# Optimization experiments

Hardware: AMD Instinct MI355X
Metric: run time of the kernel (lower is better)

The kernel has to match this reference:

```python
import jax, jax.numpy as jnp
import numpy as np

NUM_JOINTS = 24
NUM_THETAS = NUM_JOINTS * 3  # 72
NUM_VERTS = 6890
NUM_BETAS = 10
BATCH = 512

SMPL_PARENTS = np.array([0, 0, 0, 0, 1, 2, 3, 4, 5, 6, 7, 8, 9, 9, 9,
                         12, 13, 14, 16, 17, 18, 19, 20, 21], dtype=np.int32)


def setup_inputs() -> dict:
    key = jax.random.key(0)
    ks = jax.random.split(key, 6)
    x = jax.random.normal(ks[0], (BATCH, NUM_THETAS + NUM_BETAS), dtype=jnp.float32) * 0.3
    v_template = jax.random.normal(ks[1], (NUM_VERTS, 3), dtype=jnp.float32) * 0.3
    shapedirs = jax.random.normal(ks[2], (NUM_BETAS, NUM_VERTS * 3), dtype=jnp.float32) * 0.01
    posedirs = jax.random.normal(ks[3], (207, NUM_VERTS * 3), dtype=jnp.float32) * 0.001
    Jr = jax.random.uniform(ks[4], (NUM_VERTS, NUM_JOINTS), dtype=jnp.float32)
    J_regressor = Jr / jnp.sum(Jr, axis=0, keepdims=True)
    W = jax.random.uniform(ks[5], (NUM_VERTS, NUM_JOINTS), dtype=jnp.float32)
    lbs_weights = W / jnp.sum(W, axis=1, keepdims=True)  # rows sum to 1 (skinning weights)
    parents = jnp.asarray(SMPL_PARENTS)
    return {"x": x, "v_template": v_template, "shapedirs": shapedirs,
            "J_regressor": J_regressor, "posedirs": posedirs,
            "lbs_weights": lbs_weights, "parents": parents}


def batch_rodrigues(theta):
    # theta: [N,3] axis-angle -> [N,3,3] rotation matrices
    angle = jnp.linalg.norm(theta + 1e-8, axis=1, keepdims=True)  # [N,1]
    r = theta / angle                                              # [N,3] unit axis
    cos = jnp.cos(angle)[..., None]                                # [N,1,1]
    sin = jnp.sin(angle)[..., None]
    outer = r[:, :, None] * r[:, None, :]                          # [N,3,3]
    rx, ry, rz = r[:, 0], r[:, 1], r[:, 2]
    zero = jnp.zeros_like(rx)
    K = jnp.stack([zero, -rz, ry,
                   rz, zero, -rx,
                   -ry, rx, zero], axis=1).reshape(-1, 3, 3)       # skew-symmetric
    eye = jnp.eye(3, dtype=theta.dtype)
    return cos * eye + (1.0 - cos) * outer + sin * K


def global_rigid_transformation(Rs, J, parents):
    # Rs: [B,24,3,3], J: [B,24,3] -> A: [B,24,4,4]
    B = Rs.shape[0]
    dtype = Rs.dtype
    bottom = jnp.broadcast_to(jnp.array([0, 0, 0, 1], dtype=dtype), (B, 1, 4))

    def make_A(R, t):  # R:[B,3,3], t:[B,3]
        Rt = jnp.concatenate([R, t[:, :, None]], axis=2)  # [B,3,4]
        return jnp.concatenate([Rt, bottom], axis=1)       # [B,4,4]

    parents = np.asarray(parents)
    results = [make_A(Rs[:, 0], J[:, 0])]
    for i in range(1, NUM_JOINTS):
        t_rel = J[:, i] - J[:, parents[i]]
        A_here = make_A(Rs[:, i], t_rel)
        results.append(jnp.matmul(results[parents[i]], A_here))
    results = jnp.stack(results, axis=1)  # [B,24,4,4]

    Js_w0 = jnp.concatenate([J, jnp.zeros((B, NUM_JOINTS, 1), dtype=dtype)], axis=2)  # [B,24,4]
    init_bone = jnp.einsum('bjpq,bjq->bjp', results, Js_w0)                           # [B,24,4]
    A = results - jnp.pad(init_bone[..., None], ((0, 0), (0, 0), (0, 0), (3, 0)))
    return A


def reference(x, v_template, shapedirs, J_regressor, posedirs, lbs_weights, parents):
    B = x.shape[0]
    thetas = x[:, :NUM_THETAS]
    betas = x[:, NUM_THETAS:]

    # shape blendshapes
    v_shaped = (betas @ shapedirs).reshape(B, NUM_VERTS, 3) + v_template  # [B,V,3]

    J = jnp.einsum('bvc,vj->bjc', v_shaped, J_regressor)  # [B,24,3]

    # pose rotations + pose blendshapes
    Rs = batch_rodrigues(thetas.reshape(-1, 3)).reshape(B, NUM_JOINTS, 3, 3)
    pose_feature = (Rs[:, 1:] - jnp.eye(3, dtype=x.dtype)).reshape(B, 207)
    v_posed = (pose_feature @ posedirs).reshape(B, NUM_VERTS, 3) + v_shaped

    # kinematic chain
    A = global_rigid_transformation(Rs, J, parents)  # [B,24,4,4]

    # linear blend skinning
    T = jnp.einsum('vj,bjpq->bvpq', lbs_weights, A)  # [B,V,4,4]
    v_posed_homo = jnp.concatenate(
        [v_posed, jnp.ones((B, NUM_VERTS, 1), dtype=x.dtype)], axis=2)  # [B,V,4]
    verts = jnp.einsum('bvpq,bvq->bvp', T, v_posed_homo)[:, :, :3]
    return verts
```

## Files before the change

kernel.cpp:

```cpp
#include <hip/hip_runtime.h>

#define NUM_JOINTS 24
#define NUM_VERTS  6890
#define NUM_COORDS (NUM_VERTS * 3)
#define NUM_BETAS  10
#define KTOT       217
#define KPAD       224
#define BATCH      512
#define VPAD       6912

#define WS_SJP  0
#define WS_XBF  85536
#define WS_DBF  142880
#define WS_WHBF 2465312
#define WS_AH   2575904
#define WS_AL   2706976

typedef __attribute__((ext_vector_type(8))) short short8;
typedef __attribute__((ext_vector_type(4))) float f32x4;

__device__ inline unsigned short f2bf(float f) {
    union { float f; unsigned u; } c; c.f = f;
    unsigned u = c.u;
    u += 0x7fffu + ((u >> 16) & 1u);
    return (unsigned short)(u >> 16);
}
__device__ inline float bf2f(unsigned short h) {
    union { unsigned u; float f; } c; c.u = ((unsigned)h) << 16;
    return c.f;
}

struct PBShm {
    float Rs[4][24][9];
    float Jl[4][24][3];
    float Rg[4][24][9];
    float tg[4][24][3];
    float As[4][24][12];
};

__global__ __launch_bounds__(256) void k_prep(const float* __restrict__ Jr,
                                              const float* __restrict__ sd,
                                              const float* __restrict__ pd,
                                              const float* __restrict__ vt,
                                              const float* __restrict__ w,
                                              float* __restrict__ ws) {
    __shared__ __align__(16) unsigned char smem[28928];
    const int t   = blockIdx.x;
    const int tid = threadIdx.x;
    unsigned short* whbf = (unsigned short*)(ws + WS_WHBF);
    unsigned short* dbf  = (unsigned short*)(ws + WS_DBF);

    if (t < 27) {
        const int v = t * 256 + tid;
        const bool ok = (v < NUM_VERTS);
        unsigned short row[32];
        #pragma unroll
        for (int j = 0; j < 32; ++j)
            row[j] = f2bf((ok && j < 24) ? w[v * 24 + j] : 0.f);
        #pragma unroll
        for (int i = 0; i < 4; ++i)
            *(float4*)(whbf + (size_t)v * 32 + i * 8) = *(const float4*)(&row[i * 8]);
    } else if (t < 351) {
        unsigned* L = (unsigned*)smem;
        const int c0   = (t - 27) * 64;
        const int lane = tid & 63;
        const int grp  = tid >> 6;
        const int c    = c0 + lane;
        const bool cv  = (c < NUM_COORDS);
        #pragma unroll 4
        for (int i = 0; i < 28; ++i) {
            const int p  = i * 4 + grp;
            const int k0 = 2 * p, k1 = k0 + 1;
            float v0 = 0.f, v1 = 0.f;
            if (cv) {
                v0 = (k0 < 10) ? sd[(size_t)k0 * NUM_COORDS + c]
                   : (k0 < KTOT) ? pd[(size_t)(k0 - 10) * NUM_COORDS + c] : 0.f;
                v1 = (k1 < 10) ? sd[(size_t)k1 * NUM_COORDS + c]
                   : (k1 < KTOT) ? pd[(size_t)(k1 - 10) * NUM_COORDS + c] : 0.f;
            }
            L[lane * 113 + p] = (unsigned)f2bf(v0) | ((unsigned)f2bf(v1) << 16);
        }
        __syncthreads();
        #pragma unroll
        for (int i = 0; i < 7; ++i) {
            const int idx = i * 256 + tid;
            const int row = idx / 28;
            const int q   = idx % 28;
            uint4 val;
            val.x = L[row * 113 + q * 4 + 0];
            val.y = L[row * 113 + q * 4 + 1];
            val.z = L[row * 113 + q * 4 + 2];
            val.w = L[row * 113 + q * 4 + 3];
            *(uint4*)(dbf + (size_t)(c0 + row) * KPAD + q * 8) = val;
        }
    } else {
        float* Jl = (float*)smem;
        float* S  = (float*)smem + 64 * 25;
        const int strip = t - 351;
        const int v0 = strip * 64;
        #pragma unroll
        for (int i = 0; i < 6; ++i) {
            const int idx = i * 256 + tid;
            const int v = idx / 24, j = idx % 24;
            Jl[v * 25 + j] = (v0 + v < NUM_VERTS) ? Jr[(size_t)(v0 + v) * 24 + j] : 0.f;
        }
        #pragma unroll
        for (int i = 0; i < 9; ++i) {
            const int idx = i * 256 + tid;
            if (idx < 33 * 64) {
                const int s = idx / 64, v = idx % 64;
                float val = 0.f;
                if (v0 + v < NUM_VERTS) {
                    if (s < 30) val = sd[(size_t)(s / 3) * NUM_COORDS + (size_t)(v0 + v) * 3 + (s % 3)];
                    else        val = vt[(size_t)(v0 + v) * 3 + (s - 30)];
                }
                S[s * 64 + v] = val;
            }
        }
        __syncthreads();
        float* wsp = ws + WS_SJP + (size_t)strip * 792;
        for (int o = tid; o < 792; o += 256) {
            const int s = o / 24, j = o % 24;
            float sum = 0.f;
            #pragma unroll 8
            for (int v = 0; v < 64; ++v)
                sum += S[s * 64 + v] * Jl[v * 25 + j];
            wsp[o] = sum;
        }
    }
}

__global__ __launch_bounds__(256) void k_red(float* __restrict__ ws) {
    const int o = blockIdx.x * 256 + threadIdx.x;
    if (o >= 792) return;
    const float* wsp = ws + WS_SJP;
    float s0 = 0.f, s1 = 0.f, s2 = 0.f, s3 = 0.f;
    #pragma unroll
    for (int s = 0; s < 108; s += 4) {
        s0 += wsp[(size_t)(s + 0) * 792 + o];
        s1 += wsp[(size_t)(s + 1) * 792 + o];
        s2 += wsp[(size_t)(s + 2) * 792 + o];
        s3 += wsp[(size_t)(s + 3) * 792 + o];
    }
    ws[WS_SJP + o] = (s0 + s1) + (s2 + s3);
}

__global__ __launch_bounds__(256) void k_pb(const float* __restrict__ x,
                                            const int* __restrict__ parents,
                                            float* __restrict__ ws) {
    __shared__ PBShm P;
    __shared__ float SJf[792];
    unsigned short* xbf = (unsigned short*)(ws + WS_XBF);
    unsigned short* ahi = (unsigned short*)(ws + WS_AH);
    unsigned short* alo = (unsigned short*)(ws + WS_AL);
    const int tid = threadIdx.x;

    for (int o = tid; o < 792; o += 256)
        SJf[o] = ws[WS_SJP + o];
    __syncthreads();

    const int sub  = tid >> 6;
    const int lane = tid & 63;
    const int b = blockIdx.x * 4 + sub;
    const float* row = x + b * (NUM_BETAS + 72);

    if (lane < 24) {
        const int j = lane;
        const float t0 = row[3 * j + 0], t1 = row[3 * j + 1], t2 = row[3 * j + 2];
        const float a0 = t0 + 1e-8f, a1 = t1 + 1e-8f, a2 = t2 + 1e-8f;
        const float angle = sqrtf(a0 * a0 + a1 * a1 + a2 * a2);
        const float inv = 1.0f / angle;
        const float rx = t0 * inv, ry = t1 * inv, rz = t2 * inv;
        const float c = cosf(angle), sn = sinf(angle), o = 1.f - c;
        float R[9];
        R[0] = c + o * rx * rx;       R[1] = o * rx * ry - sn * rz; R[2] = o * rx * rz + sn * ry;
        R[3] = o * rx * ry + sn * rz; R[4] = c + o * ry * ry;       R[5] = o * ry * rz - sn * rx;
        R[6] = o * rx * rz - sn * ry; R[7] = o * ry * rz + sn * rx; R[8] = c + o * rz * rz;
        #pragma unroll
        for (int i = 0; i < 9; ++i) P.Rs[sub][j][i] = R[i];
        #pragma unroll
        for (int c3 = 0; c3 < 3; ++c3) {
            float s = SJf[(30 + c3) * 24 + j];
            #pragma unroll
            for (int k = 0; k < NUM_BETAS; ++k)
                s += row[72 + k] * SJf[(k * 3 + c3) * 24 + j];
            P.Jl[sub][j][c3] = s;
        }
        if (j >= 1) {
            #pragma unroll
            for (int i = 0; i < 9; ++i) {
                const float pf = R[i] - ((i == 0 || i == 4 || i == 8) ? 1.f : 0.f);
                xbf[(size_t)b * KPAD + 10 + (j - 1) * 9 + i] = f2bf(pf);
            }
        }
    }
    if (lane < NUM_BETAS) xbf[(size_t)b * KPAD + lane] = f2bf(row[72 + lane]);
    if (lane == 63) {
        #pragma unroll
        for (int k = KTOT; k < KPAD; ++k) xbf[(size_t)b * KPAD + k] = 0;
    }
    __syncthreads();

    {
        constexpr int PAR[24] = {0, 0, 0, 0, 1, 2, 3, 4, 5, 6, 7, 8,
                                 9, 9, 9, 12, 13, 14, 16, 17, 18, 19, 20, 21};
        int p = 0;
        #pragma unroll
        for (int q = 1; q < 24; ++q) if (lane == q) p = PAR[q];

        if (lane == 0) {
            #pragma unroll
            for (int q = 0; q < 9; ++q) P.Rg[sub][0][q] = P.Rs[sub][0][q];
            #pragma unroll
            for (int c3 = 0; c3 < 3; ++c3) P.tg[sub][0][c3] = P.Jl[sub][0][c3];
        }
        __syncthreads();

        #pragma unroll
        for (int lvl = 1; lvl <= 8; ++lvl) {
            constexpr unsigned LVL[9] = {0x000001u, 0x00000Eu, 0x000070u,
                                         0x000380u, 0x007C00u, 0x038000u,
                                         0x0C0000u, 0x300000u, 0xC00000u};
            if (lane < 24 && ((LVL[lvl] >> lane) & 1u)) {
                const int j = lane;
                float Rp[9], Rsl[9], tp[3];
                #pragma unroll
                for (int q = 0; q < 9; ++q) { Rp[q] = P.Rg[sub][p][q]; Rsl[q] = P.Rs[sub][j][q]; }
                #pragma unroll
                for (int r = 0; r < 3; ++r) tp[r] = P.tg[sub][p][r];
                float tmp[9];
                #pragma unroll
                for (int r = 0; r < 3; ++r)
                    #pragma unroll
                    for (int cc = 0; cc < 3; ++cc)
                        tmp[r * 3 + cc] = Rp[r * 3 + 0] * Rsl[0 + cc] +
                                          Rp[r * 3 + 1] * Rsl[3 + cc] +
                                          Rp[r * 3 + 2] * Rsl[6 + cc];
                #pragma unroll
                for (int q = 0; q < 9; ++q) P.Rg[sub][j][q] = tmp[q];
                const float tr0 = P.Jl[sub][j][0] - P.Jl[sub][p][0];
                const float tr1 = P.Jl[sub][j][1] - P.Jl[sub][p][1];
                const float tr2 = P.Jl[sub][j][2] - P.Jl[sub][p][2];
                #pragma unroll
                for (int r = 0; r < 3; ++r)
                    P.tg[sub][j][r] = Rp[r * 3 + 0] * tr0 + Rp[r * 3 + 1] * tr1 +
                                      Rp[r * 3 + 2] * tr2 + tp[r];
            }
            __syncthreads();
        }
    }

    if (lane < 24) {
        const int j = lane;
        #pragma unroll
        for (int r = 0; r < 3; ++r) {
            const float tt = P.tg[sub][j][r] - (P.Rg[sub][j][r * 3 + 0] * P.Jl[sub][j][0] +
                                                P.Rg[sub][j][r * 3 + 1] * P.Jl[sub][j][1] +
                                                P.Rg[sub][j][r * 3 + 2] * P.Jl[sub][j][2]);
            P.As[sub][j][r * 4 + 0] = P.Rg[sub][j][r * 3 + 0];
            P.As[sub][j][r * 4 + 1] = P.Rg[sub][j][r * 3 + 1];
            P.As[sub][j][r * 4 + 2] = P.Rg[sub][j][r * 3 + 2];
            P.As[sub][j][r * 4 + 3] = tt;
        }
    }
    __syncthreads();

    if (lane < 32) {
        const int r = lane >> 1;
        const int half = lane & 1;
        unsigned short hi[16], lo[16];
        #pragma unroll
        for (int i = 0; i < 16; ++i) {
            const int j = half * 16 + i;
            float v = 0.f;
            if (r < 12 && j < 24) v = P.As[sub][j][r];
            const unsigned short h = f2bf(v);
            hi[i] = h;
            lo[i] = f2bf(v - bf2f(h));
        }
        unsigned short* dh = ahi + ((size_t)b * 16 + r) * 32 + half * 16;
        unsigned short* dl = alo + ((size_t)b * 16 + r) * 32 + half * 16;
        #pragma unroll
        for (int i = 0; i < 2; ++i) {
            *(float4*)(dh + i * 8) = *(const float4*)(&hi[i * 8]);
            *(float4*)(dl + i * 8) = *(const float4*)(&lo[i * 8]);
        }
    }
}

__global__ __launch_bounds__(256, 4) void k_fused(const float* __restrict__ vt,
                                                  float* __restrict__ out,
                                                  float* __restrict__ ws) {
    __shared__ __align__(16) float VP[32 * 194];
    __shared__ __align__(16) float Tsf[4][32 * 20];

    const unsigned short* dbf  = (const unsigned short*)(ws + WS_DBF);
    const unsigned short* xbf  = (const unsigned short*)(ws + WS_XBF);
    const unsigned short* whbf = (const unsigned short*)(ws + WS_WHBF);
    const unsigned short* ahi  = (const unsigned short*)(ws + WS_AH);
    const unsigned short* alo  = (const unsigned short*)(ws + WS_AL);

    const int tid  = threadIdx.x;
    const int wave = tid >> 6;
    const int lane = tid & 63;
    const int col  = lane & 15;
    const int quad = lane >> 4;
    const int c0   = blockIdx.x * 192;
    const int b0   = blockIdx.y * 32;

    float vtl[3];
    #pragma unroll
    for (int nt = 0; nt < 3; ++nt) {
        const int nc = c0 + wave * 48 + nt * 16 + col;
        vtl[nt] = (nc < NUM_COORDS) ? vt[nc] : 0.f;
    }

    f32x4 acc[2][3] = {{{0.f,0.f,0.f,0.f},{0.f,0.f,0.f,0.f},{0.f,0.f,0.f,0.f}},
                       {{0.f,0.f,0.f,0.f},{0.f,0.f,0.f,0.f},{0.f,0.f,0.f,0.f}}};
    #pragma unroll
    for (int kb = 0; kb < 7; ++kb) {
        short8 b3[3];
        #pragma unroll
        for (int nt = 0; nt < 3; ++nt) {
            const int nc = c0 + wave * 48 + nt * 16 + col;
            b3[nt] = *(const short8*)(dbf + (size_t)nc * KPAD + quad * 8 + kb * 32);
        }
        short8 a2[2];
        #pragma unroll
        for (int mt = 0; mt < 2; ++mt)
            a2[mt] = *(const short8*)(xbf + (size_t)(b0 + mt * 16 + col) * KPAD + quad * 8 + kb * 32);
        #pragma unroll
        for (int mt = 0; mt < 2; ++mt)
            #pragma unroll
            for (int nt = 0; nt < 3; ++nt)
                acc[mt][nt] = __builtin_amdgcn_mfma_f32_16x16x32_bf16(a2[mt], b3[nt], acc[mt][nt], 0, 0, 0);
    }
    #pragma unroll
    for (int mt = 0; mt < 2; ++mt)
        #pragma unroll
        for (int nt = 0; nt < 3; ++nt) {
            const int cc = wave * 48 + nt * 16 + col;
            #pragma unroll
            for (int r = 0; r < 4; ++r)
                VP[(mt * 16 + quad * 4 + r) * 194 + cc] = acc[mt][nt][r] + vtl[nt];
        }
    __syncthreads();

    const int v0 = blockIdx.x * 64;
    short8 wfrag[4];
    #pragma unroll
    for (int mt = 0; mt < 4; ++mt)
        wfrag[mt] = *(const short8*)(whbf + (size_t)(v0 + mt * 16 + col) * 32 + quad * 8);

    float* ts = &Tsf[wave][0];
    const int vv = v0 + lane;
    const bool vok = (vv < NUM_VERTS);
    const int lhalf = lane & 31;

    for (int nt = wave; nt < 32; nt += 4) {
        const int b = b0 + nt;
        const short8 bh = *(const short8*)(ahi + ((size_t)b * 16 + col) * 32 + quad * 8);
        const short8 bl = *(const short8*)(alo + ((size_t)b * 16 + col) * 32 + quad * 8);

        f32x4 acc2[4];
        #pragma unroll
        for (int mt = 0; mt < 4; ++mt) {
            f32x4 z = {0.f, 0.f, 0.f, 0.f};
            z = __builtin_amdgcn_mfma_f32_16x16x32_bf16(wfrag[mt], bh, z, 0, 0, 0);
            z = __builtin_amdgcn_mfma_f32_16x16x32_bf16(wfrag[mt], bl, z, 0, 0, 0);
            acc2[mt] = z;
        }

        const float h0 = VP[nt * 194 + lane * 3 + 0];
        const float h1 = VP[nt * 194 + lane * 3 + 1];
        const float h2 = VP[nt * 194 + lane * 3 + 2];
        float* orow = out + (size_t)b * NUM_COORDS + (size_t)vv * 3;

        #pragma unroll
        for (int mt = 0; mt < 2; ++mt)
            #pragma unroll
            for (int r = 0; r < 4; ++r)
                ts[(mt * 16 + quad * 4 + r) * 20 + col] = acc2[mt][r];
        if (lane < 32) {
            const f32x4 t0 = *(const f32x4*)(ts + lhalf * 20 + 0);
            const f32x4 t1 = *(const f32x4*)(ts + lhalf * 20 + 4);
            const f32x4 t2 = *(const f32x4*)(ts + lhalf * 20 + 8);
            if (vok) {
                __builtin_nontemporal_store(t0[0] * h0 + t0[1] * h1 + t0[2] * h2 + t0[3], orow + 0);
                __builtin_nontemporal_store(t1[0] * h0 + t1[1] * h1 + t1[2] * h2 + t1[3], orow + 1);
                __builtin_nontemporal_store(t2[0] * h0 + t2[1] * h1 + t2[2] * h2 + t2[3], orow + 2);
            }
        }
        #pragma unroll
        for (int mt = 2; mt < 4; ++mt)
            #pragma unroll
            for (int r = 0; r < 4; ++r)
                ts[((mt - 2) * 16 + quad * 4 + r) * 20 + col] = acc2[mt][r];
        if (lane >= 32) {
            const f32x4 t0 = *(const f32x4*)(ts + lhalf * 20 + 0);
            const f32x4 t1 = *(const f32x4*)(ts + lhalf * 20 + 4);
            const f32x4 t2 = *(const f32x4*)(ts + lhalf * 20 + 8);
            if (vok) {
                __builtin_nontemporal_store(t0[0] * h0 + t0[1] * h1 + t0[2] * h2 + t0[3], orow + 0);
                __builtin_nontemporal_store(t1[0] * h0 + t1[1] * h1 + t1[2] * h2 + t1[3], orow + 1);
                __builtin_nontemporal_store(t2[0] * h0 + t2[1] * h1 + t2[2] * h2 + t2[3], orow + 2);
            }
        }
    }
}

extern "C" void kernel_launch(void* const* d_in, const int* in_sizes, int n_in,
                              void* d_out, int out_size, void* d_ws, size_t ws_size,
                              hipStream_t stream) {
    const float* x  = (const float*)d_in[0];
    const float* vt = (const float*)d_in[1];
    const float* sd = (const float*)d_in[2];
    const float* Jr = (const float*)d_in[3];
    const float* pd = (const float*)d_in[4];
    const float* w  = (const float*)d_in[5];
    const int* parents = (const int*)d_in[6];
    float* out = (float*)d_out;
    float* ws  = (float*)d_ws;

    k_prep <<<459, 256, 0, stream>>>(Jr, sd, pd, vt, w, ws);
    k_red  <<<4,   256, 0, stream>>>(ws);
    k_pb   <<<128, 256, 0, stream>>>(x, parents, ws);
    k_fused<<<dim3(108, 16), 256, 0, stream>>>(vt, out, ws);
}
```

Measured before the change: 141.7 us.

## Fold joint-regressor reduction into prep via atomics and move Rodrigues into prep

The separate k_red reduction kernel is removed. Per-strip joint-regressor partial sums are now accumulated with atomicAdd into a buffer that is zeroed by a memset. The Rodrigues rotation and pose-feature bf16 packing move out of k_pb into 48 extra k_prep blocks, which write the rotations to the workspace for k_pb to read back. This trades one kernel launch and some serial work in k_pb for a memset, atomic contention on 792 floats from 108 blocks, and non-deterministic summation order.

```diff
diff --git a/kernel.cpp b/kernel.cpp
--- a/kernel.cpp
+++ b/kernel.cpp
@@ -9,12 +9,13 @@
 #define BATCH      512
 #define VPAD       6912
 
-#define WS_SJP  0
+#define WS_SJA  0
 #define WS_XBF  85536
 #define WS_DBF  142880
 #define WS_WHBF 2465312
 #define WS_AH   2575904
 #define WS_AL   2706976
+#define WS_RS   2838048
 
 typedef __attribute__((ext_vector_type(8))) short short8;
 typedef __attribute__((ext_vector_type(4))) float f32x4;
@@ -43,12 +44,14 @@
                                               const float* __restrict__ pd,
                                               const float* __restrict__ vt,
                                               const float* __restrict__ w,
+                                              const float* __restrict__ x,
                                               float* __restrict__ ws) {
     __shared__ __align__(16) unsigned char smem[28928];
     const int t   = blockIdx.x;
     const int tid = threadIdx.x;
     unsigned short* whbf = (unsigned short*)(ws + WS_WHBF);
     unsigned short* dbf  = (unsigned short*)(ws + WS_DBF);
+    unsigned short* xbf  = (unsigned short*)(ws + WS_XBF);
 
     if (t < 27) {
         const int v = t * 256 + tid;
@@ -93,7 +96,7 @@
             val.w = L[row * 113 + q * 4 + 3];
             *(uint4*)(dbf + (size_t)(c0 + row) * KPAD + q * 8) = val;
         }
-    } else {
+    } else if (t < 459) {
         float* Jl = (float*)smem;
         float* S  = (float*)smem + 64 * 25;
         const int strip = t - 351;
@@ -118,54 +121,19 @@
             }
         }
         __syncthreads();
-        float* wsp = ws + WS_SJP + (size_t)strip * 792;
         for (int o = tid; o < 792; o += 256) {
             const int s = o / 24, j = o % 24;
             float sum = 0.f;
             #pragma unroll 8
             for (int v = 0; v < 64; ++v)
                 sum += S[s * 64 + v] * Jl[v * 25 + j];
-            wsp[o] = sum;
-        }
-    }
-}
-
-__global__ __launch_bounds__(256) void k_red(float* __restrict__ ws) {
-    const int o = blockIdx.x * 256 + threadIdx.x;
-    if (o >= 792) return;
-    const float* wsp = ws + WS_SJP;
-    float s0 = 0.f, s1 = 0.f, s2 = 0.f, s3 = 0.f;
-    #pragma unroll
-    for (int s = 0; s < 108; s += 4) {
-        s0 += wsp[(size_t)(s + 0) * 792 + o];
-        s1 += wsp[(size_t)(s + 1) * 792 + o];
-        s2 += wsp[(size_t)(s + 2) * 792 + o];
-        s3 += wsp[(size_t)(s + 3) * 792 + o];
-    }
-    ws[WS_SJP + o] = (s0 + s1) + (s2 + s3);
-}
-
-__global__ __launch_bounds__(256) void k_pb(const float* __restrict__ x,
-                                            const int* __restrict__ parents,
-                                            float* __restrict__ ws) {
-    __shared__ PBShm P;
-    __shared__ float SJf[792];
-    unsigned short* xbf = (unsigned short*)(ws + WS_XBF);
-    unsigned short* ahi = (unsigned short*)(ws + WS_AH);
-    unsigned short* alo = (unsigned short*)(ws + WS_AL);
-    const int tid = threadIdx.x;
-
-    for (int o = tid; o < 792; o += 256)
-        SJf[o] = ws[WS_SJP + o];
-    __syncthreads();
-
-    const int sub  = tid >> 6;
-    const int lane = tid & 63;
-    const int b = blockIdx.x * 4 + sub;
-    const float* row = x + b * (NUM_BETAS + 72);
-
-    if (lane < 24) {
-        const int j = lane;
+            atomicAdd(&ws[WS_SJA + o], sum);
+        }
+    } else {
+        const int idx = (t - 459) * 256 + tid;
+        const int b = idx / 24;
+        const int j = idx % 24;
+        const float* row = x + b * (NUM_BETAS + 72);
         const float t0 = row[3 * j + 0], t1 = row[3 * j + 1], t2 = row[3 * j + 2];
         const float a0 = t0 + 1e-8f, a1 = t1 + 1e-8f, a2 = t2 + 1e-8f;
         const float angle = sqrtf(a0 * a0 + a1 * a1 + a2 * a2);
@@ -176,8 +144,49 @@
         R[0] = c + o * rx * rx;       R[1] = o * rx * ry - sn * rz; R[2] = o * rx * rz + sn * ry;
         R[3] = o * rx * ry + sn * rz; R[4] = c + o * ry * ry;       R[5] = o * ry * rz - sn * rx;
         R[6] = o * rx * rz - sn * ry; R[7] = o * ry * rz + sn * rx; R[8] = c + o * rz * rz;
-        #pragma unroll
-        for (int i = 0; i < 9; ++i) P.Rs[sub][j][i] = R[i];
+        float* rsd = ws + WS_RS + (size_t)(b * 24 + j) * 9;
+        #pragma unroll
+        for (int i = 0; i < 9; ++i) rsd[i] = R[i];
+        if (j >= 1) {
+            #pragma unroll
+            for (int i = 0; i < 9; ++i) {
+                const float pf = R[i] - ((i == 0 || i == 4 || i == 8) ? 1.f : 0.f);
+                xbf[(size_t)b * KPAD + 10 + (j - 1) * 9 + i] = f2bf(pf);
+            }
+        } else {
+            #pragma unroll
+            for (int k = 0; k < NUM_BETAS; ++k)
+                xbf[(size_t)b * KPAD + k] = f2bf(row[72 + k]);
+            #pragma unroll
+            for (int k = KTOT; k < KPAD; ++k)
+                xbf[(size_t)b * KPAD + k] = 0;
+        }
+    }
+}
+
+__global__ __launch_bounds__(256) void k_pb(const float* __restrict__ x,
+                                            const int* __restrict__ parents,
+                                            float* __restrict__ ws) {
+    __shared__ PBShm P;
+    __shared__ float SJf[792];
+    unsigned short* ahi = (unsigned short*)(ws + WS_AH);
+    unsigned short* alo = (unsigned short*)(ws + WS_AL);
+    const int tid = threadIdx.x;
+
+    for (int o = tid; o < 792; o += 256)
+        SJf[o] = ws[WS_SJA + o];
+    __syncthreads();
+
+    const int sub  = tid >> 6;
+    const int lane = tid & 63;
+    const int b = blockIdx.x * 4 + sub;
+    const float* row = x + b * (NUM_BETAS + 72);
+
+    if (lane < 24) {
+        const int j = lane;
+        const float* rsd = ws + WS_RS + (size_t)(b * 24 + j) * 9;
+        #pragma unroll
+        for (int i = 0; i < 9; ++i) P.Rs[sub][j][i] = rsd[i];
         #pragma unroll
         for (int c3 = 0; c3 < 3; ++c3) {
             float s = SJf[(30 + c3) * 24 + j];
@@ -186,18 +195,6 @@
                 s += row[72 + k] * SJf[(k * 3 + c3) * 24 + j];
             P.Jl[sub][j][c3] = s;
         }
-        if (j >= 1) {
-            #pragma unroll
-            for (int i = 0; i < 9; ++i) {
-                const float pf = R[i] - ((i == 0 || i == 4 || i == 8) ? 1.f : 0.f);
-                xbf[(size_t)b * KPAD + 10 + (j - 1) * 9 + i] = f2bf(pf);
-            }
-        }
-    }
-    if (lane < NUM_BETAS) xbf[(size_t)b * KPAD + lane] = f2bf(row[72 + lane]);
-    if (lane == 63) {
-        #pragma unroll
-        for (int k = KTOT; k < KPAD; ++k) xbf[(size_t)b * KPAD + k] = 0;
     }
     __syncthreads();
 
@@ -422,8 +419,8 @@
     float* out = (float*)d_out;
     float* ws  = (float*)d_ws;
 
-    k_prep <<<459, 256, 0, stream>>>(Jr, sd, pd, vt, w, ws);
-    k_red  <<<4,   256, 0, stream>>>(ws);
+    hipMemsetAsync((void*)(ws + WS_SJA), 0, 792 * sizeof(float), stream);
+    k_prep <<<507, 256, 0, stream>>>(Jr, sd, pd, vt, w, x, ws);
     k_pb   <<<128, 256, 0, stream>>>(x, parents, ws);
     k_fused<<<dim3(108, 16), 256, 0, stream>>>(vt, out, ws);
 }
```

After: 142.9 us. About the same (+0.8%).
